# Optimization experiments

Measured on AMD Instinct MI355X. Metric: run time of the kernel, lower is better.

The kernel has to match this reference:

```python
import jax, jax.numpy as jnp
import numpy as np

HIDDEN = 3072
HEADS = 24
HEAD_DIM = HIDDEN // HEADS  # 128
MLP_HIDDEN = 4 * HIDDEN     # 12288
EPS = 1e-6


def rotate_half(x):
    # interleaved pairs: (x1, x2) -> (-x2, x1)
    xr = x.reshape(*x.shape[:-1], -1, 2)
    x1, x2 = xr[..., 0], xr[..., 1]
    return jnp.stack((-x2, x1), axis=-1).reshape(x.shape)


def rms_norm(x, gamma):
    var = jnp.mean(x * x, axis=-1, keepdims=True)
    return x * jax.lax.rsqrt(var + EPS) * gamma


def layer_norm(x):
    mu = jnp.mean(x, axis=-1, keepdims=True)
    var = jnp.mean(jnp.square(x - mu), axis=-1, keepdims=True)
    return (x - mu) * jax.lax.rsqrt(var + EPS)


def setup_inputs() -> dict:
    key = jax.random.key(0)
    ks = jax.random.split(key, 8)
    B, L_IMG, TXT = 2, 1024, 256
    L = L_IMG + TXT
    s = 0.02
    x = jax.random.normal(ks[0], (B, L, HIDDEN), jnp.float32)
    vec = jax.random.normal(ks[1], (B, HIDDEN), jnp.float32)
    w1 = jax.random.normal(ks[2], (HIDDEN, 3 * HIDDEN + MLP_HIDDEN), jnp.float32) * s
    b1 = jnp.zeros((3 * HIDDEN + MLP_HIDDEN,), jnp.float32)
    w2 = jax.random.normal(ks[3], (HIDDEN + MLP_HIDDEN, HIDDEN), jnp.float32) * s
    b2 = jnp.zeros((HIDDEN,), jnp.float32)
    wmod = jax.random.normal(ks[4], (HIDDEN, 3 * HIDDEN), jnp.float32) * s
    bmod = jnp.zeros((3 * HIDDEN,), jnp.float32)
    q_gamma = jnp.ones((HEAD_DIM,), jnp.float32)
    k_gamma = jnp.ones((HEAD_DIM,), jnp.float32)
    # real RoPE tables for the image tokens
    inv_freq = 1.0 / (10000.0 ** (np.arange(0, HEAD_DIM, 2, dtype=np.float32) / HEAD_DIM))
    angles = np.arange(L_IMG, dtype=np.float32)[:, None] * inv_freq[None, :]  # [L_img, D/2]
    freqs_cos = jnp.asarray(np.repeat(np.cos(angles), 2, axis=-1))  # [L_img, D]
    freqs_sin = jnp.asarray(np.repeat(np.sin(angles), 2, axis=-1))
    cu_seqlens_q = jnp.asarray([0, L, L, 2 * L, 2 * L], jnp.int32)  # no padding
    return {"x": x, "vec": vec, "w1": w1, "b1": b1, "w2": w2, "b2": b2,
            "wmod": wmod, "bmod": bmod, "q_gamma": q_gamma, "k_gamma": k_gamma,
            "freqs_cos": freqs_cos, "freqs_sin": freqs_sin,
            "txt_len": TXT, "cu_seqlens_q": cu_seqlens_q}


def reference(x, vec, w1, b1, w2, b2, wmod, bmod, q_gamma, k_gamma,
              freqs_cos, freqs_sin, txt_len, cu_seqlens_q):
    B, L, _ = x.shape
    # modulation: SiLU(vec) @ Wmod -> shift/scale/gate
    mod = jax.nn.silu(vec) @ wmod + bmod              # [B, 3H]
    mod_shift, mod_scale, mod_gate = jnp.split(mod, 3, axis=-1)
    x_mod = layer_norm(x) * (1.0 + mod_scale[:, None, :]) + mod_shift[:, None, :]
    h = x_mod @ w1 + b1                               # [B, L, 3H + mlp]
    qkv, mlp = h[..., :3 * HIDDEN], h[..., 3 * HIDDEN:]
    qkv = qkv.reshape(B, L, 3, HEADS, HEAD_DIM)
    q, k, v = qkv[:, :, 0], qkv[:, :, 1], qkv[:, :, 2]  # [B, L, H, D]
    q = rms_norm(q, q_gamma)
    k = rms_norm(k, k_gamma)
    # RoPE on image tokens (first L - txt_len)
    cos = freqs_cos[None, :, None, :]
    sin = freqs_sin[None, :, None, :]
    img_q, txt_q = q[:, :-txt_len], q[:, -txt_len:]
    img_k, txt_k = k[:, :-txt_len], k[:, -txt_len:]
    img_q = img_q * cos + rotate_half(img_q) * sin
    img_k = img_k * cos + rotate_half(img_k) * sin
    q = jnp.concatenate((img_q, txt_q), axis=1)
    k = jnp.concatenate((img_k, txt_k), axis=1)
    # full attention (no padding => each batch is one varlen segment)
    scale = HEAD_DIM ** -0.5
    scores = jnp.einsum("bqhd,bkhd->bhqk", q, k) * scale
    probs = jax.nn.softmax(scores, axis=-1)
    attn = jnp.einsum("bhqk,bkhd->bqhd", probs, v).reshape(B, L, HIDDEN)
    out = jnp.concatenate((attn, jax.nn.gelu(mlp, approximate=True)), axis=-1) @ w2 + b2
    return x + out * mod_gate[:, None, :]
```

## Files before the change

kernel.cpp:

```cpp
#include <hip/hip_runtime.h>

typedef unsigned short u16;
typedef unsigned int   u32;
typedef __attribute__((ext_vector_type(2))) u16 u16x2;
typedef __attribute__((ext_vector_type(4))) u16 u16x4;
typedef __attribute__((ext_vector_type(8))) u16 u16x8;
typedef __attribute__((ext_vector_type(8))) __bf16 bf16x8;
typedef __attribute__((ext_vector_type(4))) float f32x4;

#define HIDDEN 3072
#define LTOT 1280
#define BATCH 2
#define NROWS (BATCH*LTOT)
#define HEADS 24
#define HD 128
#define N1 21504
#define QKVW 9216
#define MLPW 12288
#define A2W 15360
#define EPSF 1e-6f

__device__ __forceinline__ float b2f(u16 u) {
  union { u32 i; float f; } v; v.i = ((u32)u) << 16; return v.f;
}
__device__ __forceinline__ u16 f2b(float f) {
  union { float f; u32 i; } v; v.f = f;
  u32 r = (v.i + 0x7FFFu + ((v.i >> 16) & 1u)) >> 16;
  return (u16)r;
}
__device__ __forceinline__ float lde(const void* p, size_t i, int f) {
  return f ? b2f(((const u16*)p)[i]) : ((const float*)p)[i];
}
__device__ __forceinline__ void gload16(const void* g, void* l) {
  __builtin_amdgcn_global_load_lds((const __attribute__((address_space(1))) void*)g,
                                   (__attribute__((address_space(3))) void*)l, 16, 0, 0);
}
__device__ __forceinline__ bf16x8 ldf(const u16* p) {
  return __builtin_bit_cast(bf16x8, *(const u16x8*)p);
}
__device__ __forceinline__ float gelu_tanh(float x) {
  float u = 0.7978845608028654f * (x + 0.044715f * x * x * x);
  float e = __expf(2.0f * u);
  float th = 1.0f - 2.0f / (e + 1.0f);
  return 0.5f * x * (1.0f + th);
}

__global__ void detect_kernel(const u16* __restrict__ fcos, int* __restrict__ dflag) {
  if (threadIdx.x == 0 && blockIdx.x == 0) *dflag = (fcos[0] == 0x3F80) ? 1 : 0;
}

__global__ void silu_kernel(const void* __restrict__ vec, float* __restrict__ sv,
                            const int* __restrict__ dflag) {
  int flag = *dflag;
  int i = blockIdx.x * 256 + threadIdx.x;
  if (i < BATCH * HIDDEN) { float x = lde(vec, i, flag); sv[i] = x / (1.0f + __expf(-x)); }
}

__global__ void modmul(const void* __restrict__ wmod, const float* __restrict__ sv,
                       float* __restrict__ modp, const int* __restrict__ dflag) {
  int flag = *dflag;
  int j = blockIdx.x * 256 + threadIdx.x;
  int kc = blockIdx.y;
  float a = 0.f, c = 0.f;
  int k0 = kc * 384;
  for (int k = k0; k < k0 + 384; ++k) {
    float w = lde(wmod, (size_t)k * QKVW + j, flag);
    a += sv[k] * w; c += sv[HIDDEN + k] * w;
  }
  modp[(size_t)kc * 2 * QKVW + j] = a;
  modp[(size_t)kc * 2 * QKVW + QKVW + j] = c;
}

__global__ void modred(const float* __restrict__ modp, const void* __restrict__ bmod,
                       float* __restrict__ mod, const int* __restrict__ dflag) {
  int flag = *dflag;
  int j = blockIdx.x * 256 + threadIdx.x;
  float bv = lde(bmod, j, flag);
  float a = bv, c = bv;
#pragma unroll
  for (int kc = 0; kc < 8; ++kc) {
    a += modp[(size_t)kc * 2 * QKVW + j];
    c += modp[(size_t)kc * 2 * QKVW + QKVW + j];
  }
  mod[j] = a; mod[QKVW + j] = c;
}

__global__ __launch_bounds__(256) void ln_mod_kernel(const void* __restrict__ x,
                                                     const float* __restrict__ mod,
                                                     u16* __restrict__ xmod,
                                                     const int* __restrict__ dflag) {
  int flag = *dflag;
  int row = blockIdx.x;
  int b = row / LTOT;
  int t = threadIdx.x, w = t >> 6, l = t & 63;
  float v[12], sum = 0.0f, sq = 0.0f;
  if (flag) {
    const u16* xr = (const u16*)x + (size_t)row * HIDDEN;
#pragma unroll
    for (int p = 0; p < 3; ++p) {
      u16x4 u = *(const u16x4*)&xr[p * 1024 + t * 4];
#pragma unroll
      for (int i = 0; i < 4; ++i) { float f = b2f(u[i]); v[p * 4 + i] = f; sum += f; sq += f * f; }
    }
  } else {
    const float* xr = (const float*)x + (size_t)row * HIDDEN;
#pragma unroll
    for (int p = 0; p < 3; ++p) {
      f32x4 u = *(const f32x4*)&xr[p * 1024 + t * 4];
#pragma unroll
      for (int i = 0; i < 4; ++i) { float f = u[i]; v[p * 4 + i] = f; sum += f; sq += f * f; }
    }
  }
#pragma unroll
  for (int off = 1; off < 64; off <<= 1) { sum += __shfl_xor(sum, off, 64); sq += __shfl_xor(sq, off, 64); }
  __shared__ float red[2][4];
  if (l == 0) { red[0][w] = sum; red[1][w] = sq; }
  __syncthreads();
  sum = red[0][0] + red[0][1] + red[0][2] + red[0][3];
  sq  = red[1][0] + red[1][1] + red[1][2] + red[1][3];
  float mu = sum / (float)HIDDEN;
  float var = sq / (float)HIDDEN - mu * mu;
  float rs = rsqrtf(var + EPSF);
  const float* mb = mod + (size_t)b * QKVW;
#pragma unroll
  for (int p = 0; p < 3; ++p) {
    u16x4 o;
#pragma unroll
    for (int i = 0; i < 4; ++i) {
      int col = p * 1024 + t * 4 + i;
      float y = (v[p * 4 + i] - mu) * rs;
      o[i] = f2b(y * (1.0f + mb[HIDDEN + col]) + mb[col]);
    }
    *(u16x4*)&xmod[(size_t)row * HIDDEN + p * 1024 + t * 4] = o;
  }
}

__global__ void transpose_cvt(const void* __restrict__ in, u16* __restrict__ out,
                              int R, int C, const int* __restrict__ dflag) {
  int flag = *dflag;
  __shared__ u16 tile[32][33];
  int bx = blockIdx.x * 32, by = blockIdx.y * 32;
  int tx = threadIdx.x & 31, ty = threadIdx.x >> 5;
#pragma unroll
  for (int i = 0; i < 32; i += 8)
    tile[ty + i][tx] = f2b(lde(in, (size_t)(by + ty + i) * C + bx + tx, flag));
  __syncthreads();
#pragma unroll
  for (int i = 0; i < 32; i += 8) out[(size_t)(bx + ty + i) * R + by + tx] = tile[tx][ty + i];
}

__global__ void transpose_bf16(const u16* __restrict__ in, u16* __restrict__ out,
                               int R, int C, size_t ibs, size_t obs) {
  in  += (size_t)blockIdx.z * ibs;
  out += (size_t)blockIdx.z * obs;
  __shared__ u16 tile[32][33];
  int bx = blockIdx.x * 32, by = blockIdx.y * 32;
  int tx = threadIdx.x & 31, ty = threadIdx.x >> 5;
#pragma unroll
  for (int i = 0; i < 32; i += 8) tile[ty + i][tx] = in[(size_t)(by + ty + i) * C + bx + tx];
  __syncthreads();
#pragma unroll
  for (int i = 0; i < 32; i += 8) out[(size_t)(bx + ty + i) * R + by + tx] = tile[tx][ty + i];
}

__global__ __launch_bounds__(512, 2) void gemm1_8ph(
    const u16* __restrict__ A, const u16* __restrict__ Bt,
    const void* __restrict__ bias,
    u16* __restrict__ Qb, u16* __restrict__ Kb, u16* __restrict__ Vb,
    u16* __restrict__ A2, const int* __restrict__ dflag) {
  __shared__ u16 As[2][2][256][32];
  __shared__ u16 Bs[2][2][256][32];
  constexpr int K = HIDDEN;
  constexpr int NT = K / 64;
  const int tid = threadIdx.x;
  const int l = tid & 63, w = tid >> 6;
  const int wr = w >> 2, wc = w & 3;
  const int lr = l & 15, g = l >> 4;
  const int lk_sw = (g ^ ((lr >> 1) & 3)) * 8;

  const int orig = blockIdx.x;
  const int wgid = (orig & 7) * 105 + (orig >> 3);
  const int my = wgid / 84, nx = wgid - my * 84;
  const int bm = my * 256, bn = nx * 256;

  const int row_s = tid >> 2, chunk = tid & 3;
  const int c_log = chunk ^ ((row_s >> 1) & 3);
  const u16* pa = A  + (size_t)(bm + row_s) * K + c_log * 8;
  const u16* pb = Bt + (size_t)(bn + row_s) * K + c_log * 8;

  auto stage = [&](int buf, int kk, int t) {
    const u16* sa = pa + kk * 32 + t * 64;
    const u16* sb = pb + kk * 32 + t * 64;
    u16* la = &As[buf][kk][row_s][chunk * 8];
    u16* lb = &Bs[buf][kk][row_s][chunk * 8];
    gload16(sa,                  la);
    gload16(sa + (size_t)128 * K, la + 128 * 32);
    gload16(sb,                  lb);
    gload16(sb + (size_t)128 * K, lb + 128 * 32);
  };

  f32x4 acc[8][4] = {};
  stage(0, 0, 0);
  stage(0, 1, 0);

  for (int t = 0; t < NT; ++t) {
    const int buf = t & 1;
    const bool pre = (t + 1 < NT);
    asm volatile("s_waitcnt vmcnt(4)" ::: "memory");
    __builtin_amdgcn_s_barrier();
    __builtin_amdgcn_sched_barrier(0);
    if (pre) stage(buf ^ 1, 0, t + 1);
    bf16x8 bfr[4], af[4];
#pragma unroll
    for (int fc = 0; fc < 4; ++fc) bfr[fc] = ldf(&Bs[buf][0][wc * 64 + fc * 16 + lr][lk_sw]);
#pragma unroll
    for (int j = 0; j < 4; ++j) af[j] = ldf(&As[buf][0][wr * 128 + j * 16 + lr][lk_sw]);
    __builtin_amdgcn_s_setprio(1);
#pragma unroll
    for (int j = 0; j < 4; ++j)
#pragma unroll
      for (int fc = 0; fc < 4; ++fc)
        acc[j][fc] = __builtin_amdgcn_mfma_f32_16x16x32_bf16(af[j], bfr[fc], acc[j][fc], 0, 0, 0);
    __builtin_amdgcn_s_setprio(0);
#pragma unroll
    for (int j = 0; j < 4; ++j) af[j] = ldf(&As[buf][0][wr * 128 + (4 + j) * 16 + lr][lk_sw]);
    __builtin_amdgcn_s_setprio(1);
#pragma unroll
    for (int j = 0; j < 4; ++j)
#pragma unroll
      for (int fc = 0; fc < 4; ++fc)
        acc[4 + j][fc] = __builtin_amdgcn_mfma_f32_16x16x32_bf16(af[j], bfr[fc], acc[4 + j][fc], 0, 0, 0);
    __builtin_amdgcn_s_setprio(0);
    if (pre) { asm volatile("s_waitcnt vmcnt(4)" ::: "memory"); }
    else     { asm volatile("s_waitcnt vmcnt(0)" ::: "memory"); }
    __builtin_amdgcn_s_barrier();
    __builtin_amdgcn_sched_barrier(0);
    if (pre) stage(buf ^ 1, 1, t + 1);
#pragma unroll
    for (int fc = 0; fc < 4; ++fc) bfr[fc] = ldf(&Bs[buf][1][wc * 64 + fc * 16 + lr][lk_sw]);
#pragma unroll
    for (int j = 0; j < 4; ++j) af[j] = ldf(&As[buf][1][wr * 128 + j * 16 + lr][lk_sw]);
    __builtin_amdgcn_s_setprio(1);
#pragma unroll
    for (int j = 0; j < 4; ++j)
#pragma unroll
      for (int fc = 0; fc < 4; ++fc)
        acc[j][fc] = __builtin_amdgcn_mfma_f32_16x16x32_bf16(af[j], bfr[fc], acc[j][fc], 0, 0, 0);
    __builtin_amdgcn_s_setprio(0);
#pragma unroll
    for (int j = 0; j < 4; ++j) af[j] = ldf(&As[buf][1][wr * 128 + (4 + j) * 16 + lr][lk_sw]);
    __builtin_amdgcn_s_setprio(1);
#pragma unroll
    for (int j = 0; j < 4; ++j)
#pragma unroll
      for (int fc = 0; fc < 4; ++fc)
        acc[4 + j][fc] = __builtin_amdgcn_mfma_f32_16x16x32_bf16(af[j], bfr[fc], acc[4 + j][fc], 0, 0, 0);
    __builtin_amdgcn_s_setprio(0);
  }

  const int flag = *dflag;
#pragma unroll
  for (int fr = 0; fr < 8; ++fr) {
#pragma unroll
    for (int fc = 0; fc < 4; ++fc) {
      int colg = bn + wc * 64 + fc * 16 + lr;
      float bv = lde(bias, colg, flag);
#pragma unroll
      for (int r = 0; r < 4; ++r) {
        int rowg = bm + wr * 128 + fr * 16 + g * 4 + r;
        float v = acc[fr][fc][r] + bv;
        if (colg < QKVW) {
          int which = colg / HIDDEN;
          int hd = colg - which * HIDDEN;
          int h = hd >> 7, d = hd & 127;
          int b = rowg / LTOT, pos = rowg - b * LTOT;
          u16* dst = (which == 0) ? Qb : ((which == 1) ? Kb : Vb);
          dst[(((size_t)(b * HEADS + h)) * LTOT + pos) * HD + d] = f2b(v);
        } else {
          A2[(size_t)rowg * A2W + HIDDEN + (colg - QKVW)] = f2b(gelu_tanh(v));
        }
      }
    }
  }
}

template <int MODE>
__global__ __launch_bounds__(256) void gemm_bt(
    const u16* __restrict__ A, const u16* __restrict__ Bt, int K,
    const void* __restrict__ bias,
    u16* __restrict__ out0, u16* __restrict__ out1, u16* __restrict__ out2,
    u16* __restrict__ out3, float* __restrict__ outf,
    const void* __restrict__ xin, const float* __restrict__ mod,
    const int* __restrict__ dflag) {
  __shared__ u16 As[128 * 32];
  __shared__ u16 Bs[128 * 32];
  const int flag = *dflag;
  const int t = threadIdx.x;
  const int bn = blockIdx.x * 128;
  const int bm = blockIdx.y * 128;
  const int w = t >> 6, l = t & 63;
  const int wr = (w >> 1) * 64, wc = (w & 1) * 64;
  const int lr = l & 15, lk = (l >> 4) * 8;
  f32x4 acc[4][4] = {};
  const size_t a_base = (size_t)bm * K;
  const size_t b_base = (size_t)bn * K;
  const int e0 = t * 8, e1 = e0 + 2048;
  const int r0 = e0 >> 5, c0 = e0 & 31;
  const int r1 = e1 >> 5, c1 = e1 & 31;
  const int nk = K / 32;
  for (int kt = 0; kt < nk; ++kt) {
    const int k0 = kt * 32;
    __syncthreads();
    gload16(A + a_base + (size_t)r0 * K + k0 + c0, (u16*)As + e0);
    gload16(A + a_base + (size_t)r1 * K + k0 + c1, (u16*)As + e1);
    gload16(Bt + b_base + (size_t)r0 * K + k0 + c0, (u16*)Bs + e0);
    gload16(Bt + b_base + (size_t)r1 * K + k0 + c1, (u16*)Bs + e1);
    __syncthreads();
    bf16x8 af[4], bfr[4];
#pragma unroll
    for (int i = 0; i < 4; ++i) {
      af[i]  = __builtin_bit_cast(bf16x8, *(const u16x8*)&As[(wr + i * 16 + lr) * 32 + lk]);
      bfr[i] = __builtin_bit_cast(bf16x8, *(const u16x8*)&Bs[(wc + i * 16 + lr) * 32 + lk]);
    }
#pragma unroll
    for (int i = 0; i < 4; ++i)
#pragma unroll
      for (int j = 0; j < 4; ++j)
        acc[i][j] = __builtin_amdgcn_mfma_f32_16x16x32_bf16(af[i], bfr[j], acc[i][j], 0, 0, 0);
  }
#pragma unroll
  for (int i = 0; i < 4; ++i) {
#pragma unroll
    for (int j = 0; j < 4; ++j) {
      int colg = bn + wc + j * 16 + lr;
      float bv = lde(bias, colg, flag);
#pragma unroll
      for (int r = 0; r < 4; ++r) {
        int rowg = bm + wr + i * 16 + (l >> 4) * 4 + r;
        float v = acc[i][j][r] + bv;
        if (MODE == 1) {
        } else {
          int b = rowg / LTOT;
          float gg = mod[(size_t)b * QKVW + 2 * HIDDEN + colg];
          float xv = lde(xin, (size_t)rowg * HIDDEN + colg, flag);
          outf[(size_t)rowg * HIDDEN + colg] = xv + v * gg;
        }
      }
    }
  }
}

__global__ __launch_bounds__(256) void rms_rope(
    u16* __restrict__ Qb, u16* __restrict__ Kb,
    const void* __restrict__ qg, const void* __restrict__ kg,
    const void* __restrict__ fcos, const void* __restrict__ fsin,
    const int* __restrict__ dflag) {
  int flag = *dflag;
  int w = threadIdx.x >> 6, l = threadIdx.x & 63;
  int rid = blockIdx.x * 4 + w;
  int pos = rid % LTOT;
  int d0 = 2 * l;
  size_t off = (size_t)rid * HD + d0;
  u16x2 qu = *(const u16x2*)&Qb[off];
  u16x2 ku = *(const u16x2*)&Kb[off];
  float q0 = b2f(qu[0]), q1 = b2f(qu[1]);
  float k0 = b2f(ku[0]), k1 = b2f(ku[1]);
  float sq = q0 * q0 + q1 * q1, sk = k0 * k0 + k1 * k1;
#pragma unroll
  for (int o = 1; o < 64; o <<= 1) { sq += __shfl_xor(sq, o, 64); sk += __shfl_xor(sk, o, 64); }
  float rq = rsqrtf(sq / 128.0f + EPSF), rk = rsqrtf(sk / 128.0f + EPSF);
  q0 *= rq * lde(qg, d0, flag); q1 *= rq * lde(qg, d0 + 1, flag);
  k0 *= rk * lde(kg, d0, flag); k1 *= rk * lde(kg, d0 + 1, flag);
  if (pos < 1024) {
    float cc = lde(fcos, (size_t)pos * HD + d0, flag);
    float ss = lde(fsin, (size_t)pos * HD + d0, flag);
    float nq0 = q0 * cc - q1 * ss, nq1 = q1 * cc + q0 * ss;
    float nk0 = k0 * cc - k1 * ss, nk1 = k1 * cc + k0 * ss;
    q0 = nq0; q1 = nq1; k0 = nk0; k1 = nk1;
  }
  u16x2 qo; qo[0] = f2b(q0); qo[1] = f2b(q1);
  u16x2 ko; ko[0] = f2b(k0); ko[1] = f2b(k1);
  *(u16x2*)&Qb[off] = qo;
  *(u16x2*)&Kb[off] = ko;
}

__global__ __launch_bounds__(256) void attn_kernel(
    const u16* __restrict__ Qb, const u16* __restrict__ Kb, const u16* __restrict__ Vt,
    u16* __restrict__ A2) {
  __shared__ u16 Ks[32 * 128];
  __shared__ u16 Vs[128 * 32];
  __shared__ u16 Ps[4][512];
  int t = threadIdx.x, w = t >> 6, l = t & 63;
  int bh = blockIdx.y;
  int q0 = blockIdx.x * 64 + w * 16;
  size_t base = (size_t)bh * LTOT * HD;
  int lr = l & 15, lk = (l >> 4) * 8;
  const float scale = 0.08838834764831845f;

  bf16x8 qf[4];
#pragma unroll
  for (int c = 0; c < 4; ++c)
    qf[c] = __builtin_bit_cast(bf16x8, *(const u16x8*)&Qb[base + (size_t)(q0 + lr) * HD + c * 32 + lk]);

  f32x4 o[8] = {};
  float mrun[4] = {-1e30f, -1e30f, -1e30f, -1e30f};
  float lrun[4] = {0.f, 0.f, 0.f, 0.f};

  const int e0 = t * 8, e1 = e0 + 2048;
  const int vd0 = e0 >> 5, vc0 = e0 & 31;
  const int vd1 = e1 >> 5, vc1 = e1 & 31;

  for (int kt = 0; kt < LTOT / 32; ++kt) {
    __syncthreads();
    gload16(Kb + base + (size_t)kt * 32 * HD + e0, (u16*)Ks + e0);
    gload16(Kb + base + (size_t)kt * 32 * HD + e1, (u16*)Ks + e1);
    gload16(Vt + base + (size_t)vd0 * LTOT + kt * 32 + vc0, (u16*)Vs + e0);
    gload16(Vt + base + (size_t)vd1 * LTOT + kt * 32 + vc1, (u16*)Vs + e1);
    __syncthreads();

    f32x4 s[2] = {};
#pragma unroll
    for (int sb = 0; sb < 2; ++sb)
#pragma unroll
      for (int c = 0; c < 4; ++c) {
        bf16x8 kf = __builtin_bit_cast(bf16x8, *(const u16x8*)&Ks[(sb * 16 + lr) * 128 + c * 32 + lk]);
        s[sb] = __builtin_amdgcn_mfma_f32_16x16x32_bf16(qf[c], kf, s[sb], 0, 0, 0);
      }
#pragma unroll
    for (int sb = 0; sb < 2; ++sb)
#pragma unroll
      for (int j = 0; j < 4; ++j) s[sb][j] *= scale;

#pragma unroll
    for (int j = 0; j < 4; ++j) {
      float mt = fmaxf(s[0][j], s[1][j]);
#pragma unroll
      for (int off = 1; off < 16; off <<= 1) mt = fmaxf(mt, __shfl_xor(mt, off, 64));
      float mnew = fmaxf(mrun[j], mt);
      float f = __expf(mrun[j] - mnew);
      float p0 = __expf(s[0][j] - mnew), p1 = __expf(s[1][j] - mnew);
      float ps = p0 + p1;
#pragma unroll
      for (int off = 1; off < 16; off <<= 1) ps += __shfl_xor(ps, off, 64);
      lrun[j] = lrun[j] * f + ps;
      mrun[j] = mnew;
#pragma unroll
      for (int nb = 0; nb < 8; ++nb) o[nb][j] *= f;
      int prow = (l >> 4) * 4 + j;
      Ps[w][prow * 32 + lr] = f2b(p0);
      Ps[w][prow * 32 + 16 + lr] = f2b(p1);
    }
    __syncthreads();
    bf16x8 pa = __builtin_bit_cast(bf16x8, *(const u16x8*)&Ps[w][lr * 32 + lk]);
#pragma unroll
    for (int nb = 0; nb < 8; ++nb) {
      bf16x8 vf = __builtin_bit_cast(bf16x8, *(const u16x8*)&Vs[(nb * 16 + lr) * 32 + lk]);
      o[nb] = __builtin_amdgcn_mfma_f32_16x16x32_bf16(pa, vf, o[nb], 0, 0, 0);
    }
  }

  int b = bh / HEADS, h = bh % HEADS;
#pragma unroll
  for (int j = 0; j < 4; ++j) {
    float inv = 1.0f / lrun[j];
    size_t row = (size_t)b * LTOT + q0 + (l >> 4) * 4 + j;
#pragma unroll
    for (int nb = 0; nb < 8; ++nb) {
      int col = h * HD + nb * 16 + lr;
      A2[row * A2W + col] = f2b(o[nb][j] * inv);
    }
  }
}

extern "C" void kernel_launch(void* const* d_in, const int* in_sizes, int n_in,
                              void* d_out, int out_size, void* d_ws, size_t ws_size,
                              hipStream_t stream) {
  const void* x    = d_in[0];
  const void* vec  = d_in[1];
  const void* w1   = d_in[2];
  const void* b1   = d_in[3];
  const void* w2   = d_in[4];
  const void* b2   = d_in[5];
  const void* wmod = d_in[6];
  const void* bmod = d_in[7];
  const void* qg   = d_in[8];
  const void* kg   = d_in[9];
  const void* fcos = d_in[10];
  const void* fsin = d_in[11];

  char* p = (char*)d_ws;
  int* dflag  = (int*)p; p += 256;
  float* sv   = (float*)p; p += 32768;
  float* mod  = (float*)p; p += 131072;
  float* modp = (float*)p; p += 8 * 2 * QKVW * 4;
  u16* xmod = (u16*)p; p += (size_t)NROWS * HIDDEN * 2;
  u16* w1t  = (u16*)p; p += (size_t)N1 * HIDDEN * 2;
  u16* Qb   = (u16*)p; p += (size_t)48 * LTOT * HD * 2;
  u16* Kb   = (u16*)p; p += (size_t)48 * LTOT * HD * 2;
  u16* Vb   = (u16*)p; p += (size_t)48 * LTOT * HD * 2;
  u16* Vt   = (u16*)p; p += (size_t)48 * LTOT * HD * 2;
  u16* A2   = (u16*)p; p += (size_t)NROWS * A2W * 2;
  u16* w2t  = w1t;

  detect_kernel<<<1, 64, 0, stream>>>((const u16*)fcos, dflag);
  silu_kernel<<<24, 256, 0, stream>>>(vec, sv, dflag);
  modmul<<<dim3(36, 8), 256, 0, stream>>>(wmod, sv, modp, dflag);
  modred<<<36, 256, 0, stream>>>(modp, bmod, mod, dflag);
  ln_mod_kernel<<<NROWS, 256, 0, stream>>>(x, mod, xmod, dflag);
  transpose_cvt<<<dim3(N1 / 32, HIDDEN / 32), 256, 0, stream>>>(w1, w1t, HIDDEN, N1, dflag);
  gemm1_8ph<<<(N1 / 256) * (NROWS / 256), 512, 0, stream>>>(xmod, w1t, b1,
                                                            Qb, Kb, Vb, A2, dflag);
  rms_rope<<<48 * LTOT / 4, 256, 0, stream>>>(Qb, Kb, qg, kg, fcos, fsin, dflag);
  transpose_bf16<<<dim3(HD / 32, LTOT / 32, 48), 256, 0, stream>>>(Vb, Vt, LTOT, HD,
                                                                   (size_t)LTOT * HD, (size_t)LTOT * HD);
  attn_kernel<<<dim3(LTOT / 64, 48), 256, 0, stream>>>(Qb, Kb, Vt, A2);
  transpose_cvt<<<dim3(HIDDEN / 32, A2W / 32), 256, 0, stream>>>(w2, w2t, A2W, HIDDEN, dflag);
  gemm_bt<2><<<dim3(HIDDEN / 128, NROWS / 128), 256, 0, stream>>>(A2, w2t, A2W, b2,
                                                                  nullptr, nullptr, nullptr, nullptr,
                                                                  (float*)d_out, x, mod, dflag);
}
```

Measured before the change: 1.539 ms.

## Interleave split A/B tile prefetch with MFMA phases in the fused QKV/MLP GEMM

Splits the global-to-LDS staging into separate A and B halves and issues each half between the four MFMA clusters of an iteration. LDS fragment reads are moved ahead of the global prefetches, and barriers are added around every cluster so that compute and memory phases alternate in lockstep. The aim is to spread global load issue more evenly and hide LDS read latency behind MFMA work. The cost is four times as many workgroup barriers per k-step plus extra lgkmcnt waits, which could add stalls.

```diff
diff --git a/kernel.cpp b/kernel.cpp
--- a/kernel.cpp
+++ b/kernel.cpp
@@ -188,33 +188,38 @@
   const u16* pa = A  + (size_t)(bm + row_s) * K + c_log * 8;
   const u16* pb = Bt + (size_t)(bn + row_s) * K + c_log * 8;
 
-  auto stage = [&](int buf, int kk, int t) {
+  auto stage_a = [&](int buf, int kk, int t) {
     const u16* sa = pa + kk * 32 + t * 64;
+    u16* la = &As[buf][kk][row_s][chunk * 8];
+    gload16(sa,                   la);
+    gload16(sa + (size_t)128 * K, la + 128 * 32);
+  };
+  auto stage_b = [&](int buf, int kk, int t) {
     const u16* sb = pb + kk * 32 + t * 64;
-    u16* la = &As[buf][kk][row_s][chunk * 8];
     u16* lb = &Bs[buf][kk][row_s][chunk * 8];
-    gload16(sa,                  la);
-    gload16(sa + (size_t)128 * K, la + 128 * 32);
-    gload16(sb,                  lb);
+    gload16(sb,                   lb);
     gload16(sb + (size_t)128 * K, lb + 128 * 32);
   };
 
   f32x4 acc[8][4] = {};
-  stage(0, 0, 0);
-  stage(0, 1, 0);
-
+
+  stage_a(0, 0, 0); stage_b(0, 0, 0); stage_a(0, 1, 0); stage_b(0, 1, 0);
+  asm volatile("s_waitcnt vmcnt(4)" ::: "memory");
+  __builtin_amdgcn_s_barrier();
+
+  bf16x8 af[4], bfr[4];
   for (int t = 0; t < NT; ++t) {
-    const int buf = t & 1;
+    const int b = t & 1;
     const bool pre = (t + 1 < NT);
-    asm volatile("s_waitcnt vmcnt(4)" ::: "memory");
-    __builtin_amdgcn_s_barrier();
+
+#pragma unroll
+    for (int fc = 0; fc < 4; ++fc) bfr[fc] = ldf(&Bs[b][0][wc * 64 + fc * 16 + lr][lk_sw]);
+#pragma unroll
+    for (int j = 0; j < 4; ++j) af[j] = ldf(&As[b][0][wr * 128 + j * 16 + lr][lk_sw]);
+    if (pre) stage_a(b ^ 1, 0, t + 1);
+    __builtin_amdgcn_s_barrier();
+    asm volatile("s_waitcnt lgkmcnt(0)" ::: "memory");
     __builtin_amdgcn_sched_barrier(0);
-    if (pre) stage(buf ^ 1, 0, t + 1);
-    bf16x8 bfr[4], af[4];
-#pragma unroll
-    for (int fc = 0; fc < 4; ++fc) bfr[fc] = ldf(&Bs[buf][0][wc * 64 + fc * 16 + lr][lk_sw]);
-#pragma unroll
-    for (int j = 0; j < 4; ++j) af[j] = ldf(&As[buf][0][wr * 128 + j * 16 + lr][lk_sw]);
     __builtin_amdgcn_s_setprio(1);
 #pragma unroll
     for (int j = 0; j < 4; ++j)
@@ -222,8 +227,16 @@
       for (int fc = 0; fc < 4; ++fc)
         acc[j][fc] = __builtin_amdgcn_mfma_f32_16x16x32_bf16(af[j], bfr[fc], acc[j][fc], 0, 0, 0);
     __builtin_amdgcn_s_setprio(0);
-#pragma unroll
-    for (int j = 0; j < 4; ++j) af[j] = ldf(&As[buf][0][wr * 128 + (4 + j) * 16 + lr][lk_sw]);
+    __builtin_amdgcn_s_barrier();
+
+#pragma unroll
+    for (int j = 0; j < 4; ++j) af[j] = ldf(&As[b][0][wr * 128 + (4 + j) * 16 + lr][lk_sw]);
+    if (pre) stage_b(b ^ 1, 0, t + 1);
+    if (pre) { asm volatile("s_waitcnt vmcnt(4)" ::: "memory"); }
+    else     { asm volatile("s_waitcnt vmcnt(0)" ::: "memory"); }
+    __builtin_amdgcn_s_barrier();
+    asm volatile("s_waitcnt lgkmcnt(0)" ::: "memory");
+    __builtin_amdgcn_sched_barrier(0);
     __builtin_amdgcn_s_setprio(1);
 #pragma unroll
     for (int j = 0; j < 4; ++j)
@@ -231,15 +244,16 @@
       for (int fc = 0; fc < 4; ++fc)
         acc[4 + j][fc] = __builtin_amdgcn_mfma_f32_16x16x32_bf16(af[j], bfr[fc], acc[4 + j][fc], 0, 0, 0);
     __builtin_amdgcn_s_setprio(0);
-    if (pre) { asm volatile("s_waitcnt vmcnt(4)" ::: "memory"); }
-    else     { asm volatile("s_waitcnt vmcnt(0)" ::: "memory"); }
-    __builtin_amdgcn_s_barrier();
+    __builtin_amdgcn_s_barrier();
+
+#pragma unroll
+    for (int fc = 0; fc < 4; ++fc) bfr[fc] = ldf(&Bs[b][1][wc * 64 + fc * 16 + lr][lk_sw]);
+#pragma unroll
+    for (int j = 0; j < 4; ++j) af[j] = ldf(&As[b][1][wr * 128 + j * 16 + lr][lk_sw]);
+    if (pre) stage_a(b ^ 1, 1, t + 1);
+    __builtin_amdgcn_s_barrier();
+    asm volatile("s_waitcnt lgkmcnt(0)" ::: "memory");
     __builtin_amdgcn_sched_barrier(0);
-    if (pre) stage(buf ^ 1, 1, t + 1);
-#pragma unroll
-    for (int fc = 0; fc < 4; ++fc) bfr[fc] = ldf(&Bs[buf][1][wc * 64 + fc * 16 + lr][lk_sw]);
-#pragma unroll
-    for (int j = 0; j < 4; ++j) af[j] = ldf(&As[buf][1][wr * 128 + j * 16 + lr][lk_sw]);
     __builtin_amdgcn_s_setprio(1);
 #pragma unroll
     for (int j = 0; j < 4; ++j)
@@ -247,8 +261,17 @@
       for (int fc = 0; fc < 4; ++fc)
         acc[j][fc] = __builtin_amdgcn_mfma_f32_16x16x32_bf16(af[j], bfr[fc], acc[j][fc], 0, 0, 0);
     __builtin_amdgcn_s_setprio(0);
-#pragma unroll
-    for (int j = 0; j < 4; ++j) af[j] = ldf(&As[buf][1][wr * 128 + (4 + j) * 16 + lr][lk_sw]);
+    __builtin_amdgcn_s_barrier();
+
+#pragma unroll
+    for (int j = 0; j < 4; ++j) af[j] = ldf(&As[b][1][wr * 128 + (4 + j) * 16 + lr][lk_sw]);
+    if (pre) {
+      stage_b(b ^ 1, 1, t + 1);
+      asm volatile("s_waitcnt vmcnt(4)" ::: "memory");
+    }
+    __builtin_amdgcn_s_barrier();
+    asm volatile("s_waitcnt lgkmcnt(0)" ::: "memory");
+    __builtin_amdgcn_sched_barrier(0);
     __builtin_amdgcn_s_setprio(1);
 #pragma unroll
     for (int j = 0; j < 4; ++j)
@@ -256,6 +279,7 @@
       for (int fc = 0; fc < 4; ++fc)
         acc[4 + j][fc] = __builtin_amdgcn_mfma_f32_16x16x32_bf16(af[j], bfr[fc], acc[4 + j][fc], 0, 0, 0);
     __builtin_amdgcn_s_setprio(0);
+    __builtin_amdgcn_s_barrier();
   }
 
   const int flag = *dflag;
@@ -273,9 +297,9 @@
           int which = colg / HIDDEN;
           int hd = colg - which * HIDDEN;
           int h = hd >> 7, d = hd & 127;
-          int b = rowg / LTOT, pos = rowg - b * LTOT;
+          int b2 = rowg / LTOT, pos = rowg - b2 * LTOT;
           u16* dst = (which == 0) ? Qb : ((which == 1) ? Kb : Vb);
-          dst[(((size_t)(b * HEADS + h)) * LTOT + pos) * HD + d] = f2b(v);
+          dst[(((size_t)(b2 * HEADS + h)) * LTOT + pos) * HD + d] = f2b(v);
         } else {
           A2[(size_t)rowg * A2W + HIDDEN + (colg - QKVW)] = f2b(gelu_tanh(v));
         }
```

Result: no change. 1.543 ms (+0.3%).
